# Kernel tuning notes

Measured on AMD Instinct MI355X. Metric: run time of the kernel, lower is better.

## Reference

```python
import jax, jax.numpy as jnp
import numpy as np

B, L, D_MODEL, D_STATE, D_CONV, EXPAND = 2, 1024, 1024, 16, 4, 2
D_INNER = D_MODEL * EXPAND


def setup_inputs() -> dict:
    key = jax.random.key(0)
    ks = jax.random.split(key, 8)
    s = lambda fan: 1.0 / np.sqrt(fan)
    x = jax.random.normal(ks[0], (B, L, D_MODEL), jnp.float32)
    in_proj_w = jax.random.normal(ks[1], (D_MODEL, 2 * D_INNER), jnp.float32) * s(D_MODEL)
    conv_w = jax.random.normal(ks[2], (D_INNER, 1, D_CONV), jnp.float32) * s(D_CONV)
    conv_b = jax.random.normal(ks[3], (D_INNER,), jnp.float32) * 0.01
    x_proj_w = jax.random.normal(ks[4], (D_INNER, 2 * D_STATE + D_INNER), jnp.float32) * s(D_INNER)
    dt_proj_w = jax.random.normal(ks[5], (D_INNER, D_INNER), jnp.float32) * s(D_INNER)
    dt_proj_b = jax.random.normal(ks[6], (D_INNER,), jnp.float32) * 0.01
    A_log = jnp.log(jnp.tile(jnp.arange(1, D_STATE + 1, dtype=jnp.float32)[None, :], (D_INNER, 1)))
    D = jnp.ones((D_INNER,), jnp.float32)
    out_proj_w = jax.random.normal(ks[7], (D_INNER, D_MODEL), jnp.float32) * s(D_INNER)
    return {"x": x, "in_proj_w": in_proj_w, "conv_w": conv_w, "conv_b": conv_b,
            "x_proj_w": x_proj_w, "dt_proj_w": dt_proj_w, "dt_proj_b": dt_proj_b,
            "A_log": A_log, "D": D, "out_proj_w": out_proj_w}


def _mamba_forward(x, in_proj_w, conv_w, conv_b, x_proj_w, dt_proj_w, dt_proj_b, A_log, D, out_proj_w):
    Bb, Ll, _ = x.shape
    d_inner, _, d_conv = conv_w.shape
    d_state = A_log.shape[1]
    # input projection and gate split
    xz = x @ in_proj_w                       # [B, L, 2*Di]
    x_inner, z = jnp.split(xz, 2, axis=-1)   # each [B, L, Di]
    # causal depthwise conv (left pad k-1, truncate to L == torch pad+slice)
    xc = jnp.transpose(x_inner, (0, 2, 1))   # [B, Di, L]
    xc = jax.lax.conv_general_dilated(
        xc, conv_w, window_strides=(1,), padding=[(d_conv - 1, 0)],
        dimension_numbers=("NCH", "OIH", "NCH"), feature_group_count=d_inner)
    xc = xc + conv_b[None, :, None]
    u = jax.nn.silu(jnp.transpose(xc, (0, 2, 1)))  # [B, L, Di]
    # SSM parameter projections
    ssm = u @ x_proj_w                        # [B, L, 2N+Di]
    B_ssm = ssm[..., :d_state]                # [B, L, N]
    C_ssm = ssm[..., d_state:2 * d_state]     # [B, L, N]
    dt = jax.nn.softplus(ssm[..., 2 * d_state:] @ dt_proj_w + dt_proj_b)  # [B, L, Di]
    A_real = -jnp.exp(A_log)                  # [Di, N]
    # selective scan over sequence (recurrence via lax.scan)
    def step(h, inp):
        dt_t, B_t, u_t = inp                  # [B,Di], [B,N], [B,Di]
        dA = jnp.exp(dt_t[..., None] * A_real)            # [B, Di, N]
        dBu = dt_t[..., None] * B_t[:, None, :] * u_t[..., None]
        h = dA * h + dBu
        return h, h
    h0 = jnp.zeros((Bb, d_inner, d_state), x.dtype)
    xs = (jnp.swapaxes(dt, 0, 1), jnp.swapaxes(B_ssm, 0, 1), jnp.swapaxes(u, 0, 1))
    _, states = jax.lax.scan(step, h0, xs)    # [L, B, Di, N]
    y = jnp.einsum("lbdn,lbn->lbd", states, jnp.swapaxes(C_ssm, 0, 1))
    y = jnp.swapaxes(y, 0, 1) + D * u         # skip connection
    y = y * jax.nn.silu(z)                    # gating
    return y @ out_proj_w                     # [B, L, d_model]


def reference(x, in_proj_w, conv_w, conv_b, x_proj_w, dt_proj_w, dt_proj_b, A_log, D, out_proj_w):
    return _mamba_forward(x, in_proj_w, conv_w, conv_b, x_proj_w, dt_proj_w, dt_proj_b, A_log, D, out_proj_w)
```

## Files before the change

### kernel.cpp

```cpp
#include <hip/hip_runtime.h>
#include <hip/hip_bf16.h>

#define BB 2
#define LL 1024
#define DMODEL 1024
#define DINNER 2048
#define DSTATE 16
#define DCONV 4
#define MM (BB * LL)
#define N_XZ 4096
#define N_SSM 2080
#define N_SSM_PAD 2176
#define CCH 32
#define LCH 32

typedef __hip_bfloat16 bf16;
typedef short bf16x8 __attribute__((ext_vector_type(8)));
typedef float f32x4 __attribute__((ext_vector_type(4)));

__device__ __forceinline__ void load16_lds(const bf16* g, bf16* l) {
    __builtin_amdgcn_global_load_lds(
        (const __attribute__((address_space(1))) void*)g,
        (__attribute__((address_space(3))) void*)l,
        16, 0, 0);
}

__global__ __launch_bounds__(256) void prep_kernel(
    const float* __restrict__ x, bf16* __restrict__ xbf,
    const float* __restrict__ w1, bf16* __restrict__ o1,
    const float* __restrict__ w3, bf16* __restrict__ o3,
    const float* __restrict__ w4, bf16* __restrict__ o4,
    const float* __restrict__ w2, bf16* __restrict__ w2bf,
    bf16* __restrict__ w2bc)
{
    int bid = blockIdx.x;
    if (bid >= 14464) {
        bid -= 14464;
        int i = (bid * 256 + threadIdx.x) * 4;
        float4 v = *(const float4*)(x + i);
        xbf[i + 0] = __float2bfloat16(v.x);
        xbf[i + 1] = __float2bfloat16(v.y);
        xbf[i + 2] = __float2bfloat16(v.z);
        xbf[i + 3] = __float2bfloat16(v.w);
        return;
    }
    if (bid >= 10240 && bid < 14400) {
        bid -= 10240;
        int i = (bid * 256 + threadIdx.x) * 4;
        float4 v = *(const float4*)(w2 + i);
        w2bf[i + 0] = __float2bfloat16(v.x);
        w2bf[i + 1] = __float2bfloat16(v.y);
        w2bf[i + 2] = __float2bfloat16(v.z);
        w2bf[i + 3] = __float2bfloat16(v.w);
        return;
    }
    const float* src; bf16* dst; int K, N, tn, tk, srcld;
    if (bid < 4096)        { src = w1; dst = o1; K = 1024; N = 4096; tn = bid & 127; tk = bid >> 7; srcld = N; }
    else if (bid < 8192)   { bid -= 4096; src = w3; dst = o3; K = 2048; N = 2048; tn = bid & 63; tk = bid >> 6; srcld = N; }
    else if (bid < 10240)  { bid -= 8192; src = w4; dst = o4; K = 2048; N = 1024; tn = bid & 31; tk = bid >> 5; srcld = N; }
    else                   { bid -= 14400; src = w2; dst = w2bc; K = 2048; N = 32; tn = 0; tk = bid; srcld = N_SSM; }
    __shared__ float tile[32][33];
    const int nb = tn * 32, kb = tk * 32;
    const int tx = threadIdx.x & 31, ty = threadIdx.x >> 5;
    #pragma unroll
    for (int i = 0; i < 32; i += 8) {
        int k = kb + ty + i, n = nb + tx;
        tile[ty + i][tx] = (k < K && n < N) ? src[(size_t)k * srcld + n] : 0.f;
    }
    __syncthreads();
    #pragma unroll
    for (int i = 0; i < 32; i += 8) {
        int n = nb + ty + i, k = kb + tx;
        if (n < N && k < K) dst[(size_t)n * K + k] = __float2bfloat16(tile[tx][ty + i]);
    }
}

#define TM 128
#define TN 64
#define TK 64

template<int SWZ>
__device__ __forceinline__ void remap(int id, int NX, int& bx, int& by) {
    if (SWZ >= 0) {
        int xcd = id & 7, slot = id >> 3;
        bx = (xcd << SWZ) + (slot & ((1 << SWZ) - 1));
        by = slot >> SWZ;
    } else { bx = id % NX; by = id / NX; }
}

template<int EPI>
__device__ __forceinline__ void gemm_body(
    bf16* AsB, bf16* BsB, int bx, int by,
    const bf16* __restrict__ A, int lda,
    const bf16* __restrict__ Wt, int ldw,
    float* __restrict__ Cf, bf16* __restrict__ Cb, int ldc,
    const float* __restrict__ bias,
    int N, int K, int kbeg, int Kc, bool at)
{
    const int tid = threadIdx.x;
    const int wave = tid >> 6, lane = tid & 63;
    const int wm = (wave >> 1) * 64, wn = (wave & 1) * 32;
    const int m0 = by * TM, n0 = bx * TN;
    const int lm = lane & 15, kq = lane >> 4;

    const int srow = lane >> 3;
    const int schunk = (lane & 7) ^ srow;
    const bf16* gA = A + (size_t)(m0 + wave * 32 + srow) * lda + schunk * 8;
    const bf16* gB = Wt + (size_t)(n0 + wave * 16 + srow) * ldw + schunk * 8;

    const int NK = Kc / TK;
    f32x4 acc[4][2] = {};
    const int fsw = (lm & 7);

    auto stage = [&](int buf, int it) {
        const int k0 = kbeg + it * TK;
        bf16* lA = AsB + buf * (TM * TK) + (wave * 32) * TK;
        bf16* lB = BsB + buf * (TN * TK) + (wave * 16) * TK;
        #pragma unroll
        for (int g = 0; g < 4; ++g)
            load16_lds(gA + (size_t)(8 * g) * lda + k0, lA + (8 * g) * TK);
        #pragma unroll
        for (int g = 0; g < 2; ++g)
            load16_lds(gB + (size_t)(8 * g) * ldw + k0, lB + (8 * g) * TK);
    };
    auto compute = [&](int buf) {
        const bf16* Asb = AsB + buf * (TM * TK);
        const bf16* Bsb = BsB + buf * (TN * TK);
        bf16x8 af[4][2], bfr[2][2];
        #pragma unroll
        for (int i = 0; i < 4; ++i)
            #pragma unroll
            for (int t = 0; t < 2; ++t)
                af[i][t] = *(const bf16x8*)(&Asb[(wm + i * 16 + lm) * TK + ((t * 4 + kq) ^ fsw) * 8]);
        #pragma unroll
        for (int j = 0; j < 2; ++j)
            #pragma unroll
            for (int t = 0; t < 2; ++t)
                bfr[j][t] = *(const bf16x8*)(&Bsb[(wn + j * 16 + lm) * TK + ((t * 4 + kq) ^ fsw) * 8]);
        #pragma unroll
        for (int t = 0; t < 2; ++t)
            #pragma unroll
            for (int i = 0; i < 4; ++i)
                #pragma unroll
                for (int j = 0; j < 2; ++j)
                    acc[i][j] = __builtin_amdgcn_mfma_f32_16x16x32_bf16(af[i][t], bfr[j][t], acc[i][j], 0, 0, 0);
    };

    stage(0, 0);
    for (int it = 0; it < NK; it += 2) {
        stage(1, it + 1);
        __builtin_amdgcn_s_waitcnt(0x0F76);
        __builtin_amdgcn_s_barrier();
        compute(0);
        __builtin_amdgcn_s_barrier();
        if (it + 2 < NK) {
            stage(0, it + 2);
            __builtin_amdgcn_s_waitcnt(0x0F76);
        } else {
            __builtin_amdgcn_s_waitcnt(0x0F70);
        }
        __builtin_amdgcn_s_barrier();
        compute(1);
        __builtin_amdgcn_s_barrier();
    }

    #pragma unroll
    for (int i = 0; i < 4; ++i) {
        #pragma unroll
        for (int j = 0; j < 2; ++j) {
            int gcol = n0 + wn + j * 16 + lm;
            if ((EPI == 0 || EPI == 3) && gcol >= N) continue;
            #pragma unroll
            for (int r = 0; r < 4; ++r) {
                int grow = m0 + wm + i * 16 + kq * 4 + r;
                float v = acc[i][j][r];
                if (EPI == 1) {
                    v += bias[gcol];
                    v = (v > 20.f) ? v : log1pf(__expf(v));
                    Cf[(size_t)grow * ldc + gcol] = v;
                } else if (EPI == 2) {
                    if (at) atomicAdd(&Cf[(size_t)grow * ldc + gcol], v);
                    else    Cf[(size_t)grow * ldc + gcol] = v;
                } else if (EPI == 3) {
                    if (gcol < 32) Cf[(size_t)grow * 32 + gcol] = v;
                    else           Cb[(size_t)grow * ldc + gcol] = __float2bfloat16(v);
                } else {
                    Cb[(size_t)grow * ldc + gcol] = __float2bfloat16(v);
                }
            }
        }
    }
}

template<int EPI, int KSPLIT = 1, int SWZ = -1>
__global__ __launch_bounds__(256) void mfma_gemm(
    const bf16* __restrict__ A, int lda,
    const bf16* __restrict__ Wt, int ldw,
    float* __restrict__ Cf, bf16* __restrict__ Cb, int ldc,
    const float* __restrict__ bias,
    int N, int K)
{
    __shared__ __align__(16) bf16 As[2][TM * TK];
    __shared__ __align__(16) bf16 Bs[2][TN * TK];
    int bx, by;
    if (SWZ >= 0) {
        int id = blockIdx.x + (int)(gridDim.x * blockIdx.y);
        remap<SWZ>(id, gridDim.x, bx, by);
    } else { bx = blockIdx.x; by = blockIdx.y; }
    const int Kc = K / KSPLIT;
    const int kbeg = (KSPLIT > 1) ? blockIdx.z * Kc : 0;
    gemm_body<EPI>(&As[0][0], &Bs[0][0], bx, by, A, lda, Wt, ldw, Cf, Cb, ldc,
                   bias, N, K, kbeg, Kc, KSPLIT > 1);
}

template<int EPI0, int SWZ0, int EPI1, int SWZ1>
__global__ __launch_bounds__(256) void mfma_gemm_dual(
    int nblk0, int NX0,
    const bf16* __restrict__ A0, int lda0, const bf16* __restrict__ Wt0, int ldw0,
    float* __restrict__ Cf0, bf16* __restrict__ Cb0, int ldc0,
    const float* __restrict__ bias0, int N0, int K0,
    int NX1,
    const bf16* __restrict__ A1, int lda1, const bf16* __restrict__ Wt1, int ldw1,
    float* __restrict__ Cf1, bf16* __restrict__ Cb1, int ldc1,
    const float* __restrict__ bias1, int N1, int K1)
{
    __shared__ __align__(16) bf16 As[2][TM * TK];
    __shared__ __align__(16) bf16 Bs[2][TN * TK];
    int id = blockIdx.x;
    if (id < nblk0) {
        int bx, by; remap<SWZ0>(id, NX0, bx, by);
        gemm_body<EPI0>(&As[0][0], &Bs[0][0], bx, by, A0, lda0, Wt0, ldw0,
                        Cf0, Cb0, ldc0, bias0, N0, K0, 0, K0, false);
    } else {
        id -= nblk0;
        int bx, by; remap<SWZ1>(id, NX1, bx, by);
        gemm_body<EPI1>(&As[0][0], &Bs[0][0], bx, by, A1, lda1, Wt1, ldw1,
                        Cf1, Cb1, ldc1, bias1, N1, K1, 0, K1, false);
    }
}

__global__ void conv_silu_kernel(const bf16* __restrict__ xz,
                                 const float* __restrict__ conv_w,
                                 const float* __restrict__ conv_b,
                                 bf16* __restrict__ u)
{
    int idx = blockIdx.x * blockDim.x + threadIdx.x;
    int d8 = idx & (DINNER / 8 - 1);
    int l  = (idx >> 8) & (LL - 1);
    int b  = idx >> 18;
    int d0 = d8 * 8;

    float acc[8];
    {
        float4 b0 = *(const float4*)(conv_b + d0);
        float4 b1 = *(const float4*)(conv_b + d0 + 4);
        acc[0] = b0.x; acc[1] = b0.y; acc[2] = b0.z; acc[3] = b0.w;
        acc[4] = b1.x; acc[5] = b1.y; acc[6] = b1.z; acc[7] = b1.w;
    }
    #pragma unroll
    for (int j = 0; j < DCONV; ++j) {
        int ll = l - (DCONV - 1) + j;
        if (ll >= 0) {
            bf16x8 v = *(const bf16x8*)(xz + ((size_t)(b * LL + ll)) * N_XZ + d0);
            #pragma unroll
            for (int r = 0; r < 8; ++r) {
                float xv = __uint_as_float(((unsigned)(unsigned short)v[r]) << 16);
                acc[r] = fmaf(conv_w[(d0 + r) * DCONV + j], xv, acc[r]);
            }
        }
    }
    bf16x8 out;
    #pragma unroll
    for (int r = 0; r < 8; ++r) {
        float y = acc[r] / (1.f + __expf(-acc[r]));
        bf16 h = __float2bfloat16(y);
        out[r] = *reinterpret_cast<short*>(&h);
    }
    *(bf16x8*)(u + ((size_t)(b * LL + l)) * DINNER + d0) = out;
}

__global__ __launch_bounds__(256) void scan_phase_a(
    const float* __restrict__ dt, const bf16* __restrict__ u,
    const float* __restrict__ BC,
    const float* __restrict__ A_log,
    float* __restrict__ chunkP, float* __restrict__ chunkH)
{
    const int d = blockIdx.x * 256 + threadIdx.x;
    const int c = blockIdx.y, b = blockIdx.z;
    const int l0 = c * LCH;

    float A[DSTATE];
    {
        const f32x4* ap = (const f32x4*)(A_log + d * DSTATE);
        #pragma unroll
        for (int q = 0; q < 4; ++q) {
            f32x4 v = ap[q];
            #pragma unroll
            for (int r = 0; r < 4; ++r) A[q * 4 + r] = -__expf(v[r]);
        }
    }
    float h[DSTATE];
    #pragma unroll
    for (int n = 0; n < DSTATE; ++n) h[n] = 0.f;
    float sdt = 0.f;

    const float* dtp = dt + ((size_t)b * LL + l0) * DINNER + d;
    const bf16* up = u + ((size_t)b * LL + l0) * DINNER + d;
    const float* bcp = BC + ((size_t)b * LL + l0) * 32;

    #pragma unroll 2
    for (int i = 0; i < LCH; ++i) {
        float dtv = *dtp;
        float uv  = (float)*up;
        float du  = dtv * uv;
        f32x4 Bv[4];
        #pragma unroll
        for (int q = 0; q < 4; ++q) Bv[q] = *(const f32x4*)(bcp + q * 4);
        #pragma unroll
        for (int n = 0; n < DSTATE; ++n) {
            float a = __expf(dtv * A[n]);
            h[n] = fmaf(a, h[n], du * Bv[n >> 2][n & 3]);
        }
        sdt += dtv;
        dtp += DINNER; up += DINNER; bcp += 32;
    }

    size_t idx = (((size_t)b * CCH + c) * DINNER + d) * DSTATE;
    #pragma unroll
    for (int q = 0; q < 4; ++q) {
        f32x4 pv, hv;
        #pragma unroll
        for (int r = 0; r < 4; ++r) { pv[r] = __expf(A[q * 4 + r] * sdt); hv[r] = h[q * 4 + r]; }
        *(f32x4*)(chunkP + idx + q * 4) = pv;
        *(f32x4*)(chunkH + idx + q * 4) = hv;
    }
}

__global__ __launch_bounds__(256) void scan_phase_p(
    const float* __restrict__ chunkP, float* __restrict__ chunkH)
{
    int gid = blockIdx.x * 256 + threadIdx.x;
    int n = gid & 15;
    int d = (gid >> 4) & (DINNER - 1);
    int b = gid >> 15;
    const size_t stride = (size_t)DINNER * DSTATE;
    size_t idx = ((size_t)b * CCH * DINNER + d) * DSTATE + n;
    float H = 0.f;
    for (int c = 0; c < CCH; ++c) {
        float P  = chunkP[idx];
        float hl = chunkH[idx];
        chunkH[idx] = H;
        H = fmaf(P, H, hl);
        idx += stride;
    }
}

__global__ __launch_bounds__(256) void scan_phase_b(
    const float* __restrict__ dt, bf16* __restrict__ u,
    const float* __restrict__ BC, const bf16* __restrict__ xz,
    const float* __restrict__ A_log, const float* __restrict__ Dp,
    const float* __restrict__ chunkH)
{
    const int d = blockIdx.x * 256 + threadIdx.x;
    const int c = blockIdx.y, b = blockIdx.z;
    const int l0 = c * LCH;

    float A[DSTATE];
    {
        const f32x4* ap = (const f32x4*)(A_log + d * DSTATE);
        #pragma unroll
        for (int q = 0; q < 4; ++q) {
            f32x4 v = ap[q];
            #pragma unroll
            for (int r = 0; r < 4; ++r) A[q * 4 + r] = -__expf(v[r]);
        }
    }
    const float Dd = Dp[d];
    float h[DSTATE];
    {
        size_t idx = (((size_t)b * CCH + c) * DINNER + d) * DSTATE;
        #pragma unroll
        for (int q = 0; q < 4; ++q) {
            f32x4 v = *(const f32x4*)(chunkH + idx + q * 4);
            #pragma unroll
            for (int r = 0; r < 4; ++r) h[q * 4 + r] = v[r];
        }
    }

    const float* dtp = dt + ((size_t)b * LL + l0) * DINNER + d;
    bf16* up = u + ((size_t)b * LL + l0) * DINNER + d;
    const float* bcp = BC + ((size_t)b * LL + l0) * 32;
    const bf16* zp = xz + ((size_t)b * LL + l0) * N_XZ + DINNER + d;

    #pragma unroll 2
    for (int i = 0; i < LCH; ++i) {
        float dtv = *dtp;
        float uv  = (float)*up;
        float du  = dtv * uv;
        f32x4 Bv[4], Cv[4];
        #pragma unroll
        for (int q = 0; q < 4; ++q) {
            Bv[q] = *(const f32x4*)(bcp + q * 4);
            Cv[q] = *(const f32x4*)(bcp + 16 + q * 4);
        }
        float acc = 0.f;
        #pragma unroll
        for (int n = 0; n < DSTATE; ++n) {
            float a = __expf(dtv * A[n]);
            h[n] = fmaf(a, h[n], du * Bv[n >> 2][n & 3]);
            acc = fmaf(h[n], Cv[n >> 2][n & 3], acc);
        }
        float zv = (float)*zp;
        acc = fmaf(Dd, uv, acc);
        acc *= zv / (1.f + __expf(-zv));
        *up = __float2bfloat16(acc);
        dtp += DINNER; up += DINNER; bcp += 32; zp += N_XZ;
    }
}

extern "C" void kernel_launch(void* const* d_in, const int* in_sizes, int n_in,
                              void* d_out, int out_size, void* d_ws, size_t ws_size,
                              hipStream_t stream) {
    const float* x         = (const float*)d_in[0];
    const float* in_proj_w = (const float*)d_in[1];
    const float* conv_w    = (const float*)d_in[2];
    const float* conv_b    = (const float*)d_in[3];
    const float* x_proj_w  = (const float*)d_in[4];
    const float* dt_proj_w = (const float*)d_in[5];
    const float* dt_proj_b = (const float*)d_in[6];
    const float* A_log     = (const float*)d_in[7];
    const float* Dp        = (const float*)d_in[8];
    const float* out_proj_w= (const float*)d_in[9];
    float* out = (float*)d_out;

    char* p = (char*)d_ws;
    float* dt   = (float*)p;                          p += (size_t)MM * DINNER * 4;
    bf16*  xbf  = (bf16*)dt;
    bf16*  xz   = (bf16*)p;                           p += (size_t)MM * N_XZ * 2;
    bf16*  u    = (bf16*)p;                           p += (size_t)MM * DINNER * 2;
    bf16*  wft  = (bf16*)p;                           p += (size_t)MM * N_SSM * 2;
    bf16*  Wt1  = (bf16*)p;                           p += (size_t)N_XZ * DMODEL * 2;
    bf16*  w2slot = (bf16*)p;                         p += (size_t)N_SSM_PAD * DINNER * 2;
    bf16*  W2bf = w2slot;
    bf16*  w2bc = w2slot + (size_t)DINNER * N_SSM;
    bf16*  Wt3  = (bf16*)p;                           p += (size_t)DINNER * DINNER * 2;
    bf16*  Wt4  = (bf16*)p;                           p += (size_t)DMODEL * DINNER * 2;
    float* BC   = (float*)p;                          p += (size_t)MM * 32 * 4;
    float* chunkP = (float*)Wt1;
    float* chunkH = (float*)w2slot;

    prep_kernel<<<16512, 256, 0, stream>>>(x, xbf, in_proj_w, Wt1, dt_proj_w, Wt3,
                                           out_proj_w, Wt4, x_proj_w, W2bf, w2bc);
    mfma_gemm_dual<0, 3, 0, 2><<<1536, 256, 0, stream>>>(
        1024, 64, xbf, DMODEL, Wt1, DMODEL, nullptr, xz, N_XZ, nullptr, N_XZ, DMODEL,
        32, Wt3, DINNER, W2bf + 32, N_SSM, nullptr, wft, DINNER, nullptr, DINNER, DINNER);
    {
        int n = BB * LL * DINNER / 8;
        conv_silu_kernel<<<(n + 255) / 256, 256, 0, stream>>>(xz, conv_w, conv_b, u);
    }
    mfma_gemm_dual<1, 2, 3, -1><<<528, 256, 0, stream>>>(
        512, 32, u, DINNER, wft, DINNER, dt, nullptr, DINNER, dt_proj_b, DINNER, DINNER,
        1, u, DINNER, w2bc, DINNER, BC, nullptr, 32, nullptr, 32, DINNER);
    scan_phase_a<<<dim3(DINNER / 256, CCH, BB), 256, 0, stream>>>(dt, u, BC, A_log, chunkP, chunkH);
    scan_phase_p<<<dim3(BB * DINNER * DSTATE / 256), 256, 0, stream>>>(chunkP, chunkH);
    scan_phase_b<<<dim3(DINNER / 256, CCH, BB), 256, 0, stream>>>(dt, u, BC, xz, A_log, Dp, chunkH);
    hipMemsetAsync(out, 0, (size_t)out_size * sizeof(float), stream);
    mfma_gemm<2, 4, 1><<<dim3(DMODEL / TN, MM / TM, 4), 256, 0, stream>>>(
        u, DINNER, Wt4, DINNER, out, nullptr, DMODEL, nullptr, DMODEL, DINNER);
}
```

Baseline: 334.2 us.

## Rework GEMM tiling: 256-row tiles, per-wave A staging, register-resident B fragments

Block tiles grow from 128x64 to 256x64. Each wave now stages its own 64-row A slab into private LDS, and the B (weight) fragments are loaded straight from global memory into registers with double buffering. Because no wave reads another wave's LDS, the block-wide barriers are removed, and sched_barriers are added to fix instruction ordering. The cost is more registers per wave, since each wave holds 16 accumulators plus two B fragment sets, and every wave fetches B from global memory redundantly. Grids shrink to match, and the out_proj split-K drops from 4 to 2.

```diff
diff --git a/kernel.cpp b/kernel.cpp
--- a/kernel.cpp
+++ b/kernel.cpp
@@ -75,9 +75,9 @@
     }
 }
 
-#define TM 128
-#define TN 64
-#define TK 64
+#define BTM 256
+#define WTN 64
+#define VTK 64
 
 template<int SWZ>
 __device__ __forceinline__ void remap(int id, int NX, int& bx, int& by) {
@@ -90,7 +90,8 @@
 
 template<int EPI>
 __device__ __forceinline__ void gemm_body(
-    bf16* AsB, bf16* BsB, int bx, int by,
+    bf16* AsAll,
+    int bx, int by,
     const bf16* __restrict__ A, int lda,
     const bf16* __restrict__ Wt, int ldw,
     float* __restrict__ Cf, bf16* __restrict__ Cb, int ldc,
@@ -99,80 +100,84 @@
 {
     const int tid = threadIdx.x;
     const int wave = tid >> 6, lane = tid & 63;
-    const int wm = (wave >> 1) * 64, wn = (wave & 1) * 32;
-    const int m0 = by * TM, n0 = bx * TN;
+    const int m0 = by * BTM, n0 = bx * WTN;
     const int lm = lane & 15, kq = lane >> 4;
-
-    const int srow = lane >> 3;
-    const int schunk = (lane & 7) ^ srow;
-    const bf16* gA = A + (size_t)(m0 + wave * 32 + srow) * lda + schunk * 8;
-    const bf16* gB = Wt + (size_t)(n0 + wave * 16 + srow) * ldw + schunk * 8;
-
-    const int NK = Kc / TK;
-    f32x4 acc[4][2] = {};
-    const int fsw = (lm & 7);
-
-    auto stage = [&](int buf, int it) {
-        const int k0 = kbeg + it * TK;
-        bf16* lA = AsB + buf * (TM * TK) + (wave * 32) * TK;
-        bf16* lB = BsB + buf * (TN * TK) + (wave * 16) * TK;
-        #pragma unroll
-        for (int g = 0; g < 4; ++g)
-            load16_lds(gA + (size_t)(8 * g) * lda + k0, lA + (8 * g) * TK);
-        #pragma unroll
-        for (int g = 0; g < 2; ++g)
-            load16_lds(gB + (size_t)(8 * g) * ldw + k0, lB + (8 * g) * TK);
+    const int fsw = lm & 7;
+
+    bf16* Aw = AsAll + wave * (2 * 4096);
+
+    const int sr = lane >> 3;
+    const int schunk = (lane & 7) ^ sr;
+    const bf16* gA = A + (size_t)(m0 + wave * 64 + sr) * lda + schunk * 8;
+
+    const bf16* wrow[4];
+    #pragma unroll
+    for (int j = 0; j < 4; ++j)
+        wrow[j] = Wt + (size_t)(n0 + j * 16 + lm) * ldw + kq * 8;
+
+    const int NK = Kc / VTK;
+    f32x4 acc[4][4] = {};
+    bf16x8 B0[4][2], B1[4][2];
+
+    auto stageA = [&](int buf, int it) {
+        const int k0 = kbeg + it * VTK;
+        bf16* l = Aw + buf * 4096;
+        #pragma unroll
+        for (int g = 0; g < 8; ++g)
+            load16_lds(gA + (size_t)(8 * g) * lda + k0, l + g * 512);
     };
-    auto compute = [&](int buf) {
-        const bf16* Asb = AsB + buf * (TM * TK);
-        const bf16* Bsb = BsB + buf * (TN * TK);
-        bf16x8 af[4][2], bfr[2][2];
+    auto loadB = [&](bf16x8 (&B)[4][2], int it) {
+        const int k0 = kbeg + it * VTK;
+        #pragma unroll
+        for (int j = 0; j < 4; ++j)
+            #pragma unroll
+            for (int t = 0; t < 2; ++t)
+                B[j][t] = *(const bf16x8*)(wrow[j] + k0 + t * 32);
+    };
+    auto compute = [&](int buf, bf16x8 (&B)[4][2]) {
+        const bf16* Asb = Aw + buf * 4096;
+        bf16x8 af[4][2];
         #pragma unroll
         for (int i = 0; i < 4; ++i)
             #pragma unroll
             for (int t = 0; t < 2; ++t)
-                af[i][t] = *(const bf16x8*)(&Asb[(wm + i * 16 + lm) * TK + ((t * 4 + kq) ^ fsw) * 8]);
-        #pragma unroll
-        for (int j = 0; j < 2; ++j)
-            #pragma unroll
-            for (int t = 0; t < 2; ++t)
-                bfr[j][t] = *(const bf16x8*)(&Bsb[(wn + j * 16 + lm) * TK + ((t * 4 + kq) ^ fsw) * 8]);
+                af[i][t] = *(const bf16x8*)(&Asb[(i * 16 + lm) * 64 + (((t * 4 + kq) ^ fsw) * 8)]);
         #pragma unroll
         for (int t = 0; t < 2; ++t)
             #pragma unroll
             for (int i = 0; i < 4; ++i)
                 #pragma unroll
-                for (int j = 0; j < 2; ++j)
-                    acc[i][j] = __builtin_amdgcn_mfma_f32_16x16x32_bf16(af[i][t], bfr[j][t], acc[i][j], 0, 0, 0);
+                for (int j = 0; j < 4; ++j)
+                    acc[i][j] = __builtin_amdgcn_mfma_f32_16x16x32_bf16(af[i][t], B[j][t], acc[i][j], 0, 0, 0);
     };
 
-    stage(0, 0);
+    stageA(0, 0); loadB(B0, 0);
     for (int it = 0; it < NK; it += 2) {
-        stage(1, it + 1);
-        __builtin_amdgcn_s_waitcnt(0x0F76);
-        __builtin_amdgcn_s_barrier();
-        compute(0);
-        __builtin_amdgcn_s_barrier();
+        __builtin_amdgcn_sched_barrier(0);
+        stageA(1, it + 1); loadB(B1, it + 1);
+        __builtin_amdgcn_s_waitcnt(0x4F70);
+        __builtin_amdgcn_sched_barrier(0);
+        compute(0, B0);
+        __builtin_amdgcn_sched_barrier(0);
         if (it + 2 < NK) {
-            stage(0, it + 2);
-            __builtin_amdgcn_s_waitcnt(0x0F76);
+            stageA(0, it + 2); loadB(B0, it + 2);
+            __builtin_amdgcn_s_waitcnt(0x4F70);
         } else {
             __builtin_amdgcn_s_waitcnt(0x0F70);
         }
-        __builtin_amdgcn_s_barrier();
-        compute(1);
-        __builtin_amdgcn_s_barrier();
+        __builtin_amdgcn_sched_barrier(0);
+        compute(1, B1);
     }
 
     #pragma unroll
     for (int i = 0; i < 4; ++i) {
         #pragma unroll
-        for (int j = 0; j < 2; ++j) {
-            int gcol = n0 + wn + j * 16 + lm;
+        for (int j = 0; j < 4; ++j) {
+            int gcol = n0 + j * 16 + lm;
             if ((EPI == 0 || EPI == 3) && gcol >= N) continue;
             #pragma unroll
             for (int r = 0; r < 4; ++r) {
-                int grow = m0 + wm + i * 16 + kq * 4 + r;
+                int grow = m0 + wave * 64 + i * 16 + kq * 4 + r;
                 float v = acc[i][j][r];
                 if (EPI == 1) {
                     v += bias[gcol];
@@ -193,15 +198,14 @@
 }
 
 template<int EPI, int KSPLIT = 1, int SWZ = -1>
-__global__ __launch_bounds__(256) void mfma_gemm(
+__global__ __launch_bounds__(256, 2) void mfma_gemm(
     const bf16* __restrict__ A, int lda,
     const bf16* __restrict__ Wt, int ldw,
     float* __restrict__ Cf, bf16* __restrict__ Cb, int ldc,
     const float* __restrict__ bias,
     int N, int K)
 {
-    __shared__ __align__(16) bf16 As[2][TM * TK];
-    __shared__ __align__(16) bf16 Bs[2][TN * TK];
+    __shared__ __align__(16) bf16 As[4 * 2 * 4096];
     int bx, by;
     if (SWZ >= 0) {
         int id = blockIdx.x + (int)(gridDim.x * blockIdx.y);
@@ -209,12 +213,12 @@
     } else { bx = blockIdx.x; by = blockIdx.y; }
     const int Kc = K / KSPLIT;
     const int kbeg = (KSPLIT > 1) ? blockIdx.z * Kc : 0;
-    gemm_body<EPI>(&As[0][0], &Bs[0][0], bx, by, A, lda, Wt, ldw, Cf, Cb, ldc,
+    gemm_body<EPI>(As, bx, by, A, lda, Wt, ldw, Cf, Cb, ldc,
                    bias, N, K, kbeg, Kc, KSPLIT > 1);
 }
 
 template<int EPI0, int SWZ0, int EPI1, int SWZ1>
-__global__ __launch_bounds__(256) void mfma_gemm_dual(
+__global__ __launch_bounds__(256, 2) void mfma_gemm_dual(
     int nblk0, int NX0,
     const bf16* __restrict__ A0, int lda0, const bf16* __restrict__ Wt0, int ldw0,
     float* __restrict__ Cf0, bf16* __restrict__ Cb0, int ldc0,
@@ -224,17 +228,16 @@
     float* __restrict__ Cf1, bf16* __restrict__ Cb1, int ldc1,
     const float* __restrict__ bias1, int N1, int K1)
 {
-    __shared__ __align__(16) bf16 As[2][TM * TK];
-    __shared__ __align__(16) bf16 Bs[2][TN * TK];
+    __shared__ __align__(16) bf16 As[4 * 2 * 4096];
     int id = blockIdx.x;
     if (id < nblk0) {
         int bx, by; remap<SWZ0>(id, NX0, bx, by);
-        gemm_body<EPI0>(&As[0][0], &Bs[0][0], bx, by, A0, lda0, Wt0, ldw0,
+        gemm_body<EPI0>(As, bx, by, A0, lda0, Wt0, ldw0,
                         Cf0, Cb0, ldc0, bias0, N0, K0, 0, K0, false);
     } else {
         id -= nblk0;
         int bx, by; remap<SWZ1>(id, NX1, bx, by);
-        gemm_body<EPI1>(&As[0][0], &Bs[0][0], bx, by, A1, lda1, Wt1, ldw1,
+        gemm_body<EPI1>(As, bx, by, A1, lda1, Wt1, ldw1,
                         Cf1, Cb1, ldc1, bias1, N1, K1, 0, K1, false);
     }
 }
@@ -451,20 +454,20 @@
 
     prep_kernel<<<16512, 256, 0, stream>>>(x, xbf, in_proj_w, Wt1, dt_proj_w, Wt3,
                                            out_proj_w, Wt4, x_proj_w, W2bf, w2bc);
-    mfma_gemm_dual<0, 3, 0, 2><<<1536, 256, 0, stream>>>(
-        1024, 64, xbf, DMODEL, Wt1, DMODEL, nullptr, xz, N_XZ, nullptr, N_XZ, DMODEL,
+    mfma_gemm_dual<0, 3, 0, 2><<<768, 256, 0, stream>>>(
+        512, 64, xbf, DMODEL, Wt1, DMODEL, nullptr, xz, N_XZ, nullptr, N_XZ, DMODEL,
         32, Wt3, DINNER, W2bf + 32, N_SSM, nullptr, wft, DINNER, nullptr, DINNER, DINNER);
     {
         int n = BB * LL * DINNER / 8;
         conv_silu_kernel<<<(n + 255) / 256, 256, 0, stream>>>(xz, conv_w, conv_b, u);
     }
-    mfma_gemm_dual<1, 2, 3, -1><<<528, 256, 0, stream>>>(
-        512, 32, u, DINNER, wft, DINNER, dt, nullptr, DINNER, dt_proj_b, DINNER, DINNER,
+    mfma_gemm_dual<1, 2, 3, -1><<<264, 256, 0, stream>>>(
+        256, 32, u, DINNER, wft, DINNER, dt, nullptr, DINNER, dt_proj_b, DINNER, DINNER,
         1, u, DINNER, w2bc, DINNER, BC, nullptr, 32, nullptr, 32, DINNER);
     scan_phase_a<<<dim3(DINNER / 256, CCH, BB), 256, 0, stream>>>(dt, u, BC, A_log, chunkP, chunkH);
     scan_phase_p<<<dim3(BB * DINNER * DSTATE / 256), 256, 0, stream>>>(chunkP, chunkH);
     scan_phase_b<<<dim3(DINNER / 256, CCH, BB), 256, 0, stream>>>(dt, u, BC, xz, A_log, Dp, chunkH);
     hipMemsetAsync(out, 0, (size_t)out_size * sizeof(float), stream);
-    mfma_gemm<2, 4, 1><<<dim3(DMODEL / TN, MM / TM, 4), 256, 0, stream>>>(
+    mfma_gemm<2, 2, 1><<<dim3(16, 8, 2), 256, 0, stream>>>(
         u, DINNER, Wt4, DINNER, out, nullptr, DMODEL, nullptr, DMODEL, DINNER);
 }
```

After: 392.3 us. 17.4% more time.

## Add 256x256 eight-wave MFMA GEMM with split-K and move softplus into scan

Applied to the files above, without the earlier changes.

Adds a 512-thread GEMM kernel with 256x256 tiles, a finer-grained ping-pong LDS pipeline and s_setprio around the MFMA blocks. It is used for the weight-fold and in_proj dual GEMM, for the dt projection (split-K 2 with atomics) and for out_proj (split-K 4). The dt bias and softplus move out of the GEMM epilogue into both scan phases, because split-K atomics cannot apply the nonlinearity. The BC projection becomes a separate split-K 8 atomic GEMM, which needs extra memsets of dt and BC. The aim is better data reuse and higher MFMA utilisation per tile, at the cost of atomic traffic, extra memsets and softplus being computed twice in the scan.

```diff
diff --git a/kernel.cpp b/kernel.cpp
--- a/kernel.cpp
+++ b/kernel.cpp
@@ -25,6 +25,15 @@
         16, 0, 0);
 }
 
+template<int SWZ>
+__device__ __forceinline__ void remap(int id, int NX, int& bx, int& by) {
+    if (SWZ >= 0) {
+        int xcd = id & 7, slot = id >> 3;
+        bx = (xcd << SWZ) + (slot & ((1 << SWZ) - 1));
+        by = slot >> SWZ;
+    } else { bx = id % NX; by = id / NX; }
+}
+
 __global__ __launch_bounds__(256) void prep_kernel(
     const float* __restrict__ x, bf16* __restrict__ xbf,
     const float* __restrict__ w1, bf16* __restrict__ o1,
@@ -75,47 +84,203 @@
     }
 }
 
+template<int EPI>
+__device__ __forceinline__ void gemm8_body(
+    bf16* lds, int bx, int by,
+    const bf16* __restrict__ A, int lda,
+    const bf16* __restrict__ Wt, int ldw,
+    float* __restrict__ Cf, bf16* __restrict__ Cb, int ldc,
+    int N, int K, int kbeg, int Kc)
+{
+    const int tid = threadIdx.x;
+    const int wave = tid >> 6, lane = tid & 63;
+    const int wr = wave >> 2, wc = wave & 3;
+    const int lm = lane & 15, kq = lane >> 4;
+    const int fsw = lm & 7;
+    const int m0 = by * 256, n0 = bx * 256;
+    const int NT = Kc / 64, NI = NT / 2;
+
+    const int sr = lane >> 3;
+    const int sc8 = ((lane & 7) ^ sr) * 8;
+    const bf16* gA = A  + (size_t)(m0 + wave * 16 + sr) * lda + sc8;
+    const bf16* gB = Wt + (size_t)(n0 + wave * 16 + sr) * ldw + sc8;
+
+    auto stageA = [&](int buf, int h, int t) {
+        const size_t k0 = (size_t)kbeg + (size_t)t * 64;
+        #pragma unroll
+        for (int g = 0; g < 2; ++g)
+            load16_lds(gA + (size_t)(h * 128 + g * 8) * lda + k0,
+                       lds + buf * 32768 + (h * 128 + wave * 16 + g * 8) * 64);
+    };
+    auto stageB = [&](int buf, int h, int t) {
+        const size_t k0 = (size_t)kbeg + (size_t)t * 64;
+        #pragma unroll
+        for (int g = 0; g < 2; ++g)
+            load16_lds(gB + (size_t)(h * 128 + g * 8) * ldw + k0,
+                       lds + buf * 32768 + 16384 + (h * 128 + wave * 16 + g * 8) * 64);
+    };
+
+    f32x4 acc[8][4] = {};
+    bf16x8 af[4][2], bfr[4][2];
+
+    auto readAf = [&](int buf, int qm) {
+        const bf16* Ab = lds + buf * 32768;
+        #pragma unroll
+        for (int m = 0; m < 4; ++m)
+            #pragma unroll
+            for (int ks = 0; ks < 2; ++ks)
+                af[m][ks] = *(const bf16x8*)(Ab + (wr * 128 + (qm * 4 + m) * 16 + lm) * 64
+                                                + (((ks * 4 + kq) ^ fsw) * 8));
+    };
+    auto readBf = [&](int buf, int qn) {
+        const bf16* Bb = lds + buf * 32768 + 16384;
+        #pragma unroll
+        for (int n = 0; n < 2; ++n)
+            #pragma unroll
+            for (int ks = 0; ks < 2; ++ks)
+                bfr[qn * 2 + n][ks] = *(const bf16x8*)(Bb + (wc * 64 + (qn * 2 + n) * 16 + lm) * 64
+                                                          + (((ks * 4 + kq) ^ fsw) * 8));
+    };
+    auto mfmaQ = [&](int qm, int qn) {
+        __builtin_amdgcn_s_setprio(1);
+        #pragma unroll
+        for (int ks = 0; ks < 2; ++ks)
+            #pragma unroll
+            for (int m = 0; m < 4; ++m)
+                #pragma unroll
+                for (int n = 0; n < 2; ++n)
+                    acc[qm * 4 + m][qn * 2 + n] = __builtin_amdgcn_mfma_f32_16x16x32_bf16(
+                        af[m][ks], bfr[qn * 2 + n][ks], acc[qm * 4 + m][qn * 2 + n], 0, 0, 0);
+        __builtin_amdgcn_s_setprio(0);
+    };
+    #define BAR() __builtin_amdgcn_s_barrier()
+
+    stageA(0, 0, 0); stageA(0, 1, 0);
+    stageB(0, 0, 0); stageB(0, 1, 0);
+    stageB(1, 0, 1); stageB(1, 1, 1);
+    __builtin_amdgcn_s_waitcnt(0x0F74);
+    BAR();
+
+    for (int i = 0; i < NI; ++i) {
+        const int t = 2 * i;
+        const bool lastI = (i == NI - 1);
+        stageA(1, 0, t + 1);
+        readAf(0, 0); readBf(0, 0);
+        BAR(); mfmaQ(0, 0); BAR();
+        stageA(1, 1, t + 1);
+        readBf(0, 1);
+        BAR(); mfmaQ(0, 1); BAR();
+        if (!lastI) stageB(0, 0, t + 2);
+        readAf(0, 1);
+        BAR(); mfmaQ(1, 0); BAR();
+        if (!lastI) { stageB(0, 1, t + 2); __builtin_amdgcn_s_waitcnt(0x0F74); }
+        else        { __builtin_amdgcn_s_waitcnt(0x0F70); }
+        BAR(); mfmaQ(1, 1); BAR();
+        if (!lastI) stageA(0, 0, t + 2);
+        readAf(1, 0); readBf(1, 0);
+        BAR(); mfmaQ(0, 0); BAR();
+        if (!lastI) stageA(0, 1, t + 2);
+        readBf(1, 1);
+        BAR(); mfmaQ(0, 1); BAR();
+        if (!lastI) stageB(1, 0, t + 3);
+        readAf(1, 1);
+        BAR(); mfmaQ(1, 0); BAR();
+        if (!lastI) { stageB(1, 1, t + 3); __builtin_amdgcn_s_waitcnt(0x0F74); }
+        BAR(); mfmaQ(1, 1); BAR();
+    }
+    #undef BAR
+
+    #pragma unroll
+    for (int i = 0; i < 8; ++i) {
+        #pragma unroll
+        for (int j = 0; j < 4; ++j) {
+            int gcol = n0 + wc * 64 + j * 16 + lm;
+            if (EPI == 0 && gcol >= N) continue;
+            #pragma unroll
+            for (int r = 0; r < 4; ++r) {
+                int grow = m0 + wr * 128 + i * 16 + kq * 4 + r;
+                float v = acc[i][j][r];
+                if (EPI == 2) atomicAdd(&Cf[(size_t)grow * ldc + gcol], v);
+                else          Cb[(size_t)grow * ldc + gcol] = __float2bfloat16(v);
+            }
+        }
+    }
+}
+
+template<int EPI, int KSPLIT, int SWZ>
+__global__ __launch_bounds__(512, 2) void mfma8_gemm(
+    const bf16* __restrict__ A, int lda,
+    const bf16* __restrict__ Wt, int ldw,
+    float* __restrict__ Cf, bf16* __restrict__ Cb, int ldc,
+    int N, int K)
+{
+    __shared__ __align__(16) bf16 lds[4 * 16384];
+    int bx, by;
+    if (SWZ >= 0) {
+        int id = blockIdx.x + (int)(gridDim.x * blockIdx.y);
+        remap<SWZ>(id, gridDim.x, bx, by);
+    } else { bx = blockIdx.x; by = blockIdx.y; }
+    const int Kc = K / KSPLIT;
+    const int kbeg = (KSPLIT > 1) ? blockIdx.z * Kc : 0;
+    gemm8_body<EPI>(lds, bx, by, A, lda, Wt, ldw, Cf, Cb, ldc, N, K, kbeg, Kc);
+}
+
+__global__ __launch_bounds__(512, 2) void mfma8_dual(
+    const bf16* __restrict__ A0, int lda0, const bf16* __restrict__ Wt0, int ldw0,
+    bf16* __restrict__ Cb0, int ldc0, int N0, int K0,
+    const bf16* __restrict__ A1, int lda1, const bf16* __restrict__ Wt1, int ldw1,
+    bf16* __restrict__ Cb1, int ldc1, int N1, int K1)
+{
+    __shared__ __align__(16) bf16 lds[4 * 16384];
+    int id = blockIdx.x;
+    const bf16 *A, *Wt; bf16* Cb; int lda, ldw, ldc, N, K, bx, by;
+    if (id < 64) {
+        remap<0>(id, 8, bx, by);
+        A = A0; lda = lda0; Wt = Wt0; ldw = ldw0; Cb = Cb0; ldc = ldc0; N = N0; K = K0;
+    } else {
+        remap<1>(id - 64, 16, bx, by);
+        A = A1; lda = lda1; Wt = Wt1; ldw = ldw1; Cb = Cb1; ldc = ldc1; N = N1; K = K1;
+    }
+    gemm8_body<0>(lds, bx, by, A, lda, Wt, ldw, nullptr, Cb, ldc, N, K, 0, K);
+}
+
 #define TM 128
 #define TN 64
 #define TK 64
-
-template<int SWZ>
-__device__ __forceinline__ void remap(int id, int NX, int& bx, int& by) {
-    if (SWZ >= 0) {
-        int xcd = id & 7, slot = id >> 3;
-        bx = (xcd << SWZ) + (slot & ((1 << SWZ) - 1));
-        by = slot >> SWZ;
-    } else { bx = id % NX; by = id / NX; }
-}
-
-template<int EPI>
-__device__ __forceinline__ void gemm_body(
-    bf16* AsB, bf16* BsB, int bx, int by,
+template<int EPI, int KSPLIT = 1, int SWZ = -1>
+__global__ __launch_bounds__(256) void mfma_gemm(
     const bf16* __restrict__ A, int lda,
     const bf16* __restrict__ Wt, int ldw,
     float* __restrict__ Cf, bf16* __restrict__ Cb, int ldc,
     const float* __restrict__ bias,
-    int N, int K, int kbeg, int Kc, bool at)
-{
+    int N, int K)
+{
+    __shared__ __align__(16) bf16 As[2][TM * TK];
+    __shared__ __align__(16) bf16 Bs[2][TN * TK];
     const int tid = threadIdx.x;
     const int wave = tid >> 6, lane = tid & 63;
     const int wm = (wave >> 1) * 64, wn = (wave & 1) * 32;
+    int bx, by;
+    if (SWZ >= 0) {
+        int id = blockIdx.x + (int)(gridDim.x * blockIdx.y);
+        remap<SWZ>(id, gridDim.x, bx, by);
+    } else { bx = blockIdx.x; by = blockIdx.y; }
     const int m0 = by * TM, n0 = bx * TN;
     const int lm = lane & 15, kq = lane >> 4;
-
     const int srow = lane >> 3;
     const int schunk = (lane & 7) ^ srow;
     const bf16* gA = A + (size_t)(m0 + wave * 32 + srow) * lda + schunk * 8;
     const bf16* gB = Wt + (size_t)(n0 + wave * 16 + srow) * ldw + schunk * 8;
-
+    const int Kc = K / KSPLIT;
+    const int kbeg = (KSPLIT > 1) ? blockIdx.z * Kc : 0;
     const int NK = Kc / TK;
     f32x4 acc[4][2] = {};
     const int fsw = (lm & 7);
 
     auto stage = [&](int buf, int it) {
         const int k0 = kbeg + it * TK;
-        bf16* lA = AsB + buf * (TM * TK) + (wave * 32) * TK;
-        bf16* lB = BsB + buf * (TN * TK) + (wave * 16) * TK;
+        bf16* lA = &As[buf][(wave * 32) * TK];
+        bf16* lB = &Bs[buf][(wave * 16) * TK];
         #pragma unroll
         for (int g = 0; g < 4; ++g)
             load16_lds(gA + (size_t)(8 * g) * lda + k0, lA + (8 * g) * TK);
@@ -124,19 +289,17 @@
             load16_lds(gB + (size_t)(8 * g) * ldw + k0, lB + (8 * g) * TK);
     };
     auto compute = [&](int buf) {
-        const bf16* Asb = AsB + buf * (TM * TK);
-        const bf16* Bsb = BsB + buf * (TN * TK);
         bf16x8 af[4][2], bfr[2][2];
         #pragma unroll
         for (int i = 0; i < 4; ++i)
             #pragma unroll
             for (int t = 0; t < 2; ++t)
-                af[i][t] = *(const bf16x8*)(&Asb[(wm + i * 16 + lm) * TK + ((t * 4 + kq) ^ fsw) * 8]);
+                af[i][t] = *(const bf16x8*)(&As[buf][(wm + i * 16 + lm) * TK + ((t * 4 + kq) ^ fsw) * 8]);
         #pragma unroll
         for (int j = 0; j < 2; ++j)
             #pragma unroll
             for (int t = 0; t < 2; ++t)
-                bfr[j][t] = *(const bf16x8*)(&Bsb[(wn + j * 16 + lm) * TK + ((t * 4 + kq) ^ fsw) * 8]);
+                bfr[j][t] = *(const bf16x8*)(&Bs[buf][(wn + j * 16 + lm) * TK + ((t * 4 + kq) ^ fsw) * 8]);
         #pragma unroll
         for (int t = 0; t < 2; ++t)
             #pragma unroll
@@ -169,73 +332,16 @@
         #pragma unroll
         for (int j = 0; j < 2; ++j) {
             int gcol = n0 + wn + j * 16 + lm;
-            if ((EPI == 0 || EPI == 3) && gcol >= N) continue;
+            if ((EPI == 0 || EPI == 4) && gcol >= N) continue;
             #pragma unroll
             for (int r = 0; r < 4; ++r) {
                 int grow = m0 + wm + i * 16 + kq * 4 + r;
                 float v = acc[i][j][r];
-                if (EPI == 1) {
-                    v += bias[gcol];
-                    v = (v > 20.f) ? v : log1pf(__expf(v));
-                    Cf[(size_t)grow * ldc + gcol] = v;
-                } else if (EPI == 2) {
-                    if (at) atomicAdd(&Cf[(size_t)grow * ldc + gcol], v);
-                    else    Cf[(size_t)grow * ldc + gcol] = v;
-                } else if (EPI == 3) {
-                    if (gcol < 32) Cf[(size_t)grow * 32 + gcol] = v;
-                    else           Cb[(size_t)grow * ldc + gcol] = __float2bfloat16(v);
-                } else {
-                    Cb[(size_t)grow * ldc + gcol] = __float2bfloat16(v);
-                }
+                if (EPI == 4)      atomicAdd(&Cf[(size_t)grow * 32 + gcol], v);
+                else if (EPI == 2) atomicAdd(&Cf[(size_t)grow * ldc + gcol], v);
+                else               Cb[(size_t)grow * ldc + gcol] = __float2bfloat16(v);
             }
         }
-    }
-}
-
-template<int EPI, int KSPLIT = 1, int SWZ = -1>
-__global__ __launch_bounds__(256) void mfma_gemm(
-    const bf16* __restrict__ A, int lda,
-    const bf16* __restrict__ Wt, int ldw,
-    float* __restrict__ Cf, bf16* __restrict__ Cb, int ldc,
-    const float* __restrict__ bias,
-    int N, int K)
-{
-    __shared__ __align__(16) bf16 As[2][TM * TK];
-    __shared__ __align__(16) bf16 Bs[2][TN * TK];
-    int bx, by;
-    if (SWZ >= 0) {
-        int id = blockIdx.x + (int)(gridDim.x * blockIdx.y);
-        remap<SWZ>(id, gridDim.x, bx, by);
-    } else { bx = blockIdx.x; by = blockIdx.y; }
-    const int Kc = K / KSPLIT;
-    const int kbeg = (KSPLIT > 1) ? blockIdx.z * Kc : 0;
-    gemm_body<EPI>(&As[0][0], &Bs[0][0], bx, by, A, lda, Wt, ldw, Cf, Cb, ldc,
-                   bias, N, K, kbeg, Kc, KSPLIT > 1);
-}
-
-template<int EPI0, int SWZ0, int EPI1, int SWZ1>
-__global__ __launch_bounds__(256) void mfma_gemm_dual(
-    int nblk0, int NX0,
-    const bf16* __restrict__ A0, int lda0, const bf16* __restrict__ Wt0, int ldw0,
-    float* __restrict__ Cf0, bf16* __restrict__ Cb0, int ldc0,
-    const float* __restrict__ bias0, int N0, int K0,
-    int NX1,
-    const bf16* __restrict__ A1, int lda1, const bf16* __restrict__ Wt1, int ldw1,
-    float* __restrict__ Cf1, bf16* __restrict__ Cb1, int ldc1,
-    const float* __restrict__ bias1, int N1, int K1)
-{
-    __shared__ __align__(16) bf16 As[2][TM * TK];
-    __shared__ __align__(16) bf16 Bs[2][TN * TK];
-    int id = blockIdx.x;
-    if (id < nblk0) {
-        int bx, by; remap<SWZ0>(id, NX0, bx, by);
-        gemm_body<EPI0>(&As[0][0], &Bs[0][0], bx, by, A0, lda0, Wt0, ldw0,
-                        Cf0, Cb0, ldc0, bias0, N0, K0, 0, K0, false);
-    } else {
-        id -= nblk0;
-        int bx, by; remap<SWZ1>(id, NX1, bx, by);
-        gemm_body<EPI1>(&As[0][0], &Bs[0][0], bx, by, A1, lda1, Wt1, ldw1,
-                        Cf1, Cb1, ldc1, bias1, N1, K1, 0, K1, false);
     }
 }
 
@@ -281,8 +387,8 @@
 
 __global__ __launch_bounds__(256) void scan_phase_a(
     const float* __restrict__ dt, const bf16* __restrict__ u,
-    const float* __restrict__ BC,
-    const float* __restrict__ A_log,
+    const float* __restrict__ BC, const float* __restrict__ A_log,
+    const float* __restrict__ dtb,
     float* __restrict__ chunkP, float* __restrict__ chunkH)
 {
     const int d = blockIdx.x * 256 + threadIdx.x;
@@ -299,6 +405,7 @@
             for (int r = 0; r < 4; ++r) A[q * 4 + r] = -__expf(v[r]);
         }
     }
+    const float bd = dtb[d];
     float h[DSTATE];
     #pragma unroll
     for (int n = 0; n < DSTATE; ++n) h[n] = 0.f;
@@ -310,7 +417,8 @@
 
     #pragma unroll 2
     for (int i = 0; i < LCH; ++i) {
-        float dtv = *dtp;
+        float dtv = *dtp + bd;
+        dtv = (dtv > 20.f) ? dtv : log1pf(__expf(dtv));
         float uv  = (float)*up;
         float du  = dtv * uv;
         f32x4 Bv[4];
@@ -359,6 +467,7 @@
     const float* __restrict__ dt, bf16* __restrict__ u,
     const float* __restrict__ BC, const bf16* __restrict__ xz,
     const float* __restrict__ A_log, const float* __restrict__ Dp,
+    const float* __restrict__ dtb,
     const float* __restrict__ chunkH)
 {
     const int d = blockIdx.x * 256 + threadIdx.x;
@@ -376,6 +485,7 @@
         }
     }
     const float Dd = Dp[d];
+    const float bd = dtb[d];
     float h[DSTATE];
     {
         size_t idx = (((size_t)b * CCH + c) * DINNER + d) * DSTATE;
@@ -394,7 +504,8 @@
 
     #pragma unroll 2
     for (int i = 0; i < LCH; ++i) {
-        float dtv = *dtp;
+        float dtv = *dtp + bd;
+        dtv = (dtv > 20.f) ? dtv : log1pf(__expf(dtv));
         float uv  = (float)*up;
         float du  = dtv * uv;
         f32x4 Bv[4], Cv[4];
@@ -451,20 +562,23 @@
 
     prep_kernel<<<16512, 256, 0, stream>>>(x, xbf, in_proj_w, Wt1, dt_proj_w, Wt3,
                                            out_proj_w, Wt4, x_proj_w, W2bf, w2bc);
-    mfma_gemm_dual<0, 3, 0, 2><<<1536, 256, 0, stream>>>(
-        1024, 64, xbf, DMODEL, Wt1, DMODEL, nullptr, xz, N_XZ, nullptr, N_XZ, DMODEL,
-        32, Wt3, DINNER, W2bf + 32, N_SSM, nullptr, wft, DINNER, nullptr, DINNER, DINNER);
+    mfma8_dual<<<192, 512, 0, stream>>>(
+        Wt3, DINNER, W2bf + 32, N_SSM, wft, DINNER, DINNER, DINNER,
+        xbf, DMODEL, Wt1, DMODEL, xz, N_XZ, N_XZ, DMODEL);
+    hipMemsetAsync(dt, 0, (size_t)MM * DINNER * 4, stream);
+    hipMemsetAsync(BC, 0, (size_t)MM * 32 * 4, stream);
+    hipMemsetAsync(out, 0, (size_t)out_size * sizeof(float), stream);
     {
         int n = BB * LL * DINNER / 8;
         conv_silu_kernel<<<(n + 255) / 256, 256, 0, stream>>>(xz, conv_w, conv_b, u);
     }
-    mfma_gemm_dual<1, 2, 3, -1><<<528, 256, 0, stream>>>(
-        512, 32, u, DINNER, wft, DINNER, dt, nullptr, DINNER, dt_proj_b, DINNER, DINNER,
-        1, u, DINNER, w2bc, DINNER, BC, nullptr, 32, nullptr, 32, DINNER);
-    scan_phase_a<<<dim3(DINNER / 256, CCH, BB), 256, 0, stream>>>(dt, u, BC, A_log, chunkP, chunkH);
+    mfma8_gemm<2, 2, 0><<<dim3(8, 8, 2), 512, 0, stream>>>(
+        u, DINNER, wft, DINNER, dt, nullptr, DINNER, DINNER, DINNER);
+    mfma_gemm<4, 8, -1><<<dim3(1, 16, 8), 256, 0, stream>>>(
+        u, DINNER, w2bc, DINNER, BC, nullptr, 32, nullptr, 32, DINNER);
+    scan_phase_a<<<dim3(DINNER / 256, CCH, BB), 256, 0, stream>>>(dt, u, BC, A_log, dt_proj_b, chunkP, chunkH);
     scan_phase_p<<<dim3(BB * DINNER * DSTATE / 256), 256, 0, stream>>>(chunkP, chunkH);
-    scan_phase_b<<<dim3(DINNER / 256, CCH, BB), 256, 0, stream>>>(dt, u, BC, xz, A_log, Dp, chunkH);
-    hipMemsetAsync(out, 0, (size_t)out_size * sizeof(float), stream);
-    mfma_gemm<2, 4, 1><<<dim3(DMODEL / TN, MM / TM, 4), 256, 0, stream>>>(
-        u, DINNER, Wt4, DINNER, out, nullptr, DMODEL, nullptr, DMODEL, DINNER);
-}
+    scan_phase_b<<<dim3(DINNER / 256, CCH, BB), 256, 0, stream>>>(dt, u, BC, xz, A_log, Dp, dt_proj_b, chunkH);
+    mfma8_gemm<2, 4, -1><<<dim3(4, 8, 4), 512, 0, stream>>>(
+        u, DINNER, Wt4, DINNER, out, nullptr, DMODEL, DMODEL, DINNER);
+}
```

After: 405.2 us. 1.21x slower.
